# Optimization experiments

Hardware: AMD Instinct MI355X
Metric: run time of the kernel (lower is better)

## Reference

```python
import jax, jax.numpy as jnp
import numpy as np

B, S, D = 2, 2048, 512
E, H, TOP_K = 8, 1024, 2
SCALE = 1.0


def setup_inputs() -> dict:
    key = jax.random.key(0)
    ks = jax.random.split(key, 7)
    s = lambda fan_in: 1.0 / np.sqrt(fan_in)
    return {
        "x": jax.random.normal(ks[0], (B, S, D), dtype=jnp.float32),
        "gate_w": jax.random.normal(ks[1], (E, D), dtype=jnp.float32) * s(D),
        "w1": jax.random.normal(ks[2], (E, H, D), dtype=jnp.float32) * s(D),
        "w2": jax.random.normal(ks[3], (E, D, H), dtype=jnp.float32) * s(H),
        "sg_gate": jax.random.normal(ks[4], (H, D), dtype=jnp.float32) * s(D),
        "sg_up": jax.random.normal(ks[5], (H, D), dtype=jnp.float32) * s(D),
        "sg_down": jax.random.normal(ks[6], (D, H), dtype=jnp.float32) * s(H),
    }


def reference(x, gate_w, w1, w2, sg_gate, sg_up, sg_down):
    b, s_len, d = x.shape
    xf = x.reshape(-1, d)                      # [N, D]
    n = xf.shape[0]

    # --- TopKRouter: logits -> top-k -> softmax over the k selected logits ---
    logits = (xf @ gate_w.T) * SCALE           # [N, E]
    topk_w, idx = jax.lax.top_k(logits, TOP_K)  # [N, K]
    topk_w = jax.nn.softmax(topk_w, axis=-1)
    # per-token combine weights scattered to expert slots: [N, E]
    comb = jnp.zeros((n, E), dtype=xf.dtype).at[jnp.arange(n)[:, None], idx].add(topk_w)

    # --- Routed experts (dense masked compute; weight 0 for unrouted) ---
    h = jax.nn.silu(jnp.einsum('td,ehd->teh', xf, w1))   # [N, E, H]
    eo = jnp.einsum('teh,edh->ted', h, w2)               # [N, E, D]
    routed = jnp.einsum('te,ted->td', comb, eo)          # [N, D]

    # --- Shared expert (SwiGLU), n_shared_experts = 1 ---
    shared = (jax.nn.silu(xf @ sg_gate.T) * (xf @ sg_up.T)) @ sg_down.T

    return (routed + shared).reshape(b, s_len, d)
```

## Files before the change

### kernel.cpp

```cpp
#include <hip/hip_runtime.h>
#include <hip/hip_bf16.h>


#define NTOK 4096
#define DDIM 512
#define HDIM 1024
#define NEXP 8
#define CAP  4096

typedef unsigned short u16;
typedef __attribute__((ext_vector_type(8))) short short8;
typedef __attribute__((ext_vector_type(4))) float f32x4;

__device__ __forceinline__ u16 f2bf(float f) {
  unsigned u = __float_as_uint(f);
  u += 0x7fffu + ((u >> 16) & 1u);
  return (u16)(u >> 16);
}
__device__ __forceinline__ float bf2f(u16 v) {
  return __uint_as_float(((unsigned)v) << 16);
}
__device__ __forceinline__ float silu_f(float v) { return v / (1.0f + __expf(-v)); }

__device__ __forceinline__ void gload16(const u16* g, u16* l) {
  __builtin_amdgcn_global_load_lds((const __attribute__((address_space(1))) void*)g,
                                   (__attribute__((address_space(3))) void*)l, 16, 0, 0);
}

__global__ __launch_bounds__(256) void prep(
    const float* __restrict__ x,   const float* __restrict__ gw,
    const float* __restrict__ w1,  const float* __restrict__ w2,
    const float* __restrict__ sgg, const float* __restrict__ sgu,
    const float* __restrict__ sgd,
    u16* __restrict__ Xb, u16* __restrict__ W1b, u16* __restrict__ W2b,
    u16* __restrict__ SGGb, u16* __restrict__ SGUb, u16* __restrict__ SGDb,
    int* __restrict__ tIdx, float2* __restrict__ tW) {
  if (blockIdx.x < NTOK / 4) {
    const int lane = threadIdx.x & 63;
    const int wid  = threadIdx.x >> 6;
    const int t = blockIdx.x * 4 + wid;
    const float4* xr = (const float4*)(x + (size_t)t * DDIM + lane * 8);
    const float4 x0 = xr[0], x1 = xr[1];
    short8 xbv;
    xbv[0]=f2bf(x0.x); xbv[1]=f2bf(x0.y); xbv[2]=f2bf(x0.z); xbv[3]=f2bf(x0.w);
    xbv[4]=f2bf(x1.x); xbv[5]=f2bf(x1.y); xbv[6]=f2bf(x1.z); xbv[7]=f2bf(x1.w);
    *(short8*)&Xb[(size_t)t * DDIM + lane * 8] = xbv;
    float p[NEXP];
#pragma unroll
    for (int e = 0; e < NEXP; ++e) {
      const float4* gr = (const float4*)(gw + (size_t)e * DDIM + lane * 8);
      const float4 g0 = gr[0], g1 = gr[1];
      p[e] = x0.x*g0.x + x0.y*g0.y + x0.z*g0.z + x0.w*g0.w +
             x1.x*g1.x + x1.y*g1.y + x1.z*g1.z + x1.w*g1.w;
    }
#pragma unroll
    for (int e = 0; e < NEXP; ++e) {
#pragma unroll
      for (int m = 32; m >= 1; m >>= 1) p[e] += __shfl_xor(p[e], m);
    }
    if (lane == 0) {
      int i0 = 0; float v0 = p[0];
#pragma unroll
      for (int e = 1; e < NEXP; ++e) if (p[e] > v0) { v0 = p[e]; i0 = e; }
      int i1 = -1; float v1 = -3.0e38f;
#pragma unroll
      for (int e = 0; e < NEXP; ++e) if (e != i0 && p[e] > v1) { v1 = p[e]; i1 = e; }
      const float ex1 = __expf(v1 - v0);
      const float inv = 1.0f / (1.0f + ex1);
      tIdx[t] = i0 | (i1 << 4);
      tW[t] = make_float2(inv, ex1 * inv);
    }
  } else {
    constexpr int NW1 = NEXP * HDIM * DDIM / 4;
    constexpr int NSG = HDIM * DDIM / 4;
    constexpr int TOT = 2 * NW1 + 3 * NSG;
    int i = (blockIdx.x - NTOK / 4) * 256 + threadIdx.x;
    const int stride = (gridDim.x - NTOK / 4) * 256;
    for (; i < TOT; i += stride) {
      const float* s; u16* d; int j = i;
      if (j < NW1)               { s = w1;  d = W1b;  }
      else if ((j -= NW1) < NW1) { s = w2;  d = W2b;  }
      else if ((j -= NW1) < NSG) { s = sgg; d = SGGb; }
      else if ((j -= NSG) < NSG) { s = sgu; d = SGUb; }
      else        { j -= NSG;      s = sgd; d = SGDb; }
      float4 v = ((const float4*)s)[j];
      ushort4 o;
      o.x = f2bf(v.x); o.y = f2bf(v.y); o.z = f2bf(v.z); o.w = f2bf(v.w);
      ((ushort4*)d)[j] = o;
    }
  }
}

__global__ __launch_bounds__(256) void build_lists(
    const int* __restrict__ tIdx,
    int* __restrict__ counts, int* __restrict__ elist) {
  const int e = blockIdx.x;
  __shared__ int cnt;
  if (threadIdx.x == 0) cnt = 0;
  __syncthreads();
  const int lane = threadIdx.x & 63;
  int* el = elist + e * CAP;
  for (int base = 0; base < NTOK; base += 256) {
    const int t = base + threadIdx.x;
    const int pk = tIdx[t];
#pragma unroll
    for (int slot = 0; slot < 2; ++slot) {
      const bool m = (((pk >> (slot * 4)) & 15) == e);
      const unsigned long long b = __ballot(m);
      const int my  = __popcll(b & ((1ull << lane) - 1));
      const int tot = __popcll(b);
      int wbase = 0;
      if (lane == 0 && tot) wbase = atomicAdd(&cnt, tot);
      wbase = __shfl(wbase, 0);
      if (m) el[wbase + my] = t * 2 + slot;
    }
  }
  __syncthreads();
  if (threadIdx.x == 0) counts[e] = cnt;
}

#define BUFE (128 * 32)

__global__ __launch_bounds__(512, 6) void gemm_up(
    const u16* __restrict__ Xb, const u16* __restrict__ W1b,
    const u16* __restrict__ SGGb, const u16* __restrict__ SGUb,
    u16* __restrict__ Hbuf, u16* __restrict__ ACT,
    const int* __restrict__ counts, const int* __restrict__ elist) {
  constexpr int KDIM = DDIM, KSTEP = KDIM / 32;
  const int z = blockIdx.z;
  const int m0 = blockIdx.y * 128;
  const bool routed = (z < NEXP);

  int mlim; const u16* Bp = nullptr; const int* lst = nullptr;
  if (routed) {
    if (blockIdx.x >= 8) return;
    mlim = counts[z];
    lst = elist + z * CAP;
    Bp = W1b + (size_t)z * HDIM * KDIM;
  } else {
    mlim = NTOK;
  }
  if (m0 >= mlim) return;

  __shared__ __align__(16) u16 As[3 * BUFE];
  __shared__ __align__(16) u16 Bs[3 * BUFE];
  __shared__ int rowE[128];

  const int tid = threadIdx.x;
  const int wid = tid >> 6, lane = tid & 63;

  if (routed) {
    if (tid < 128) {
      int idx = m0 + tid; if (idx > mlim - 1) idx = mlim - 1;
      rowE[tid] = lst[idx];
    }
    __syncthreads();
  }

  const int row = tid >> 2;
  const int kcp = ((tid & 3) - ((row >> 1) & 3)) & 3;
  const int arow = routed ? (rowE[row] >> 1) : (m0 + row);
  const u16* aG = Xb + (size_t)arow * KDIM + kcp * 8;
  const u16* bG;
  if (routed) {
    bG = Bp + (size_t)(blockIdx.x * 128 + row) * KDIM + kcp * 8;
  } else {
    const int n0 = blockIdx.x * 64;
    bG = (row < 64) ? SGGb + (size_t)(n0 + row) * KDIM + kcp * 8
                    : SGUb + (size_t)(n0 + row - 64) * KDIM + kcp * 8;
  }

  const int lr = lane & 15, lk = lane >> 4;
  const int rslot = ((lk + ((lr >> 1) & 3)) & 3) * 8;

  auto STAGE = [&](int kt, int c) {
    gload16(aG + kt * 32, As + c * BUFE + tid * 8);
    gload16(bG + kt * 32, Bs + c * BUFE + tid * 8);
  };

  const f32x4 zero = {0.f, 0.f, 0.f, 0.f};

  if (routed) {
    const int n0 = blockIdx.x * 128;
    const int wm = (wid >> 2) * 64, wn = (wid & 3) * 32;
    f32x4 acc[4][2];
#pragma unroll
    for (int i = 0; i < 4; ++i)
#pragma unroll
      for (int j = 0; j < 2; ++j) acc[i][j] = zero;

    STAGE(0, 0); STAGE(1, 1);
    for (int kt = 0; kt < KSTEP; ++kt) {
      if (kt + 1 < KSTEP) asm volatile("s_waitcnt vmcnt(2)" ::: "memory");
      else                asm volatile("s_waitcnt vmcnt(0)" ::: "memory");
      __builtin_amdgcn_s_barrier();
      __builtin_amdgcn_sched_barrier(0);
      if (kt + 2 < KSTEP) STAGE(kt + 2, (kt + 2) % 3);
      const u16* ab = As + (kt % 3) * BUFE;
      const u16* bb = Bs + (kt % 3) * BUFE;
      short8 a[4], b[2];
#pragma unroll
      for (int i = 0; i < 4; ++i)
        a[i] = *(const short8*)&ab[(wm + i * 16 + lr) * 32 + rslot];
#pragma unroll
      for (int j = 0; j < 2; ++j)
        b[j] = *(const short8*)&bb[(wn + j * 16 + lr) * 32 + rslot];
      __builtin_amdgcn_s_setprio(1);
#pragma unroll
      for (int i = 0; i < 4; ++i)
#pragma unroll
        for (int j = 0; j < 2; ++j)
          acc[i][j] = __builtin_amdgcn_mfma_f32_16x16x32_bf16(a[i], b[j], acc[i][j], 0, 0, 0);
      __builtin_amdgcn_s_setprio(0);
    }

#pragma unroll
    for (int i = 0; i < 4; ++i) {
#pragma unroll
      for (int j = 0; j < 2; ++j) {
        const int col = n0 + wn + j * 16 + lr;
#pragma unroll
        for (int r = 0; r < 4; ++r) {
          const int m = wm + i * 16 + lk * 4 + r;
          if (m0 + m < mlim)
            Hbuf[(size_t)rowE[m] * HDIM + col] = f2bf(silu_f(acc[i][j][r]));
        }
      }
    }
  } else {
    const int n0 = blockIdx.x * 64;
    const int wm = (wid >> 2) * 64, ws = (wid & 3) * 16;
    f32x4 ag[4], au[4];
#pragma unroll
    for (int i = 0; i < 4; ++i) { ag[i] = zero; au[i] = zero; }

    STAGE(0, 0); STAGE(1, 1);
    for (int kt = 0; kt < KSTEP; ++kt) {
      if (kt + 1 < KSTEP) asm volatile("s_waitcnt vmcnt(2)" ::: "memory");
      else                asm volatile("s_waitcnt vmcnt(0)" ::: "memory");
      __builtin_amdgcn_s_barrier();
      __builtin_amdgcn_sched_barrier(0);
      if (kt + 2 < KSTEP) STAGE(kt + 2, (kt + 2) % 3);
      const u16* ab = As + (kt % 3) * BUFE;
      const u16* bb = Bs + (kt % 3) * BUFE;
      short8 a[4], bg, bu;
#pragma unroll
      for (int i = 0; i < 4; ++i)
        a[i] = *(const short8*)&ab[(wm + i * 16 + lr) * 32 + rslot];
      bg = *(const short8*)&bb[(ws + lr) * 32 + rslot];
      bu = *(const short8*)&bb[(64 + ws + lr) * 32 + rslot];
      __builtin_amdgcn_s_setprio(1);
#pragma unroll
      for (int i = 0; i < 4; ++i) {
        ag[i] = __builtin_amdgcn_mfma_f32_16x16x32_bf16(a[i], bg, ag[i], 0, 0, 0);
        au[i] = __builtin_amdgcn_mfma_f32_16x16x32_bf16(a[i], bu, au[i], 0, 0, 0);
      }
      __builtin_amdgcn_s_setprio(0);
    }

#pragma unroll
    for (int i = 0; i < 4; ++i) {
      const int col = n0 + ws + lr;
#pragma unroll
      for (int r = 0; r < 4; ++r) {
        const int m = wm + i * 16 + lk * 4 + r;
        ACT[(size_t)(m0 + m) * HDIM + col] = f2bf(silu_f(ag[i][r]) * au[i][r]);
      }
    }
  }
}

__global__ __launch_bounds__(512, 6) void gemm_down(
    const u16* __restrict__ Hbuf, const u16* __restrict__ W2b,
    const u16* __restrict__ ACT,  const u16* __restrict__ SGDb,
    u16* __restrict__ eo0, u16* __restrict__ eo1,
    float* __restrict__ sh0, float* __restrict__ sh1,
    const int* __restrict__ counts, const int* __restrict__ elist) {
  constexpr int KFULL = HDIM;
  constexpr int KSTEP = 512 / 32;
  const int z = blockIdx.z;
  const int n0 = blockIdx.x * 128;
  const int m0 = blockIdx.y * 128;
  const bool routed = (z < 2 * NEXP);
  const int khalf = routed ? (z & 1) : (z - 2 * NEXP);
  const int koff = khalf * 512;

  int mlim; const u16* Ap; const u16* Bp; const int* lst = nullptr;
  if (routed) {
    const int e = z >> 1;
    mlim = counts[e];
    lst = elist + e * CAP;
    Ap = Hbuf;
    Bp = W2b + (size_t)e * DDIM * KFULL;
  } else {
    mlim = NTOK;
    Ap = ACT;
    Bp = SGDb;
  }
  if (m0 >= mlim) return;

  __shared__ __align__(16) u16 As[3 * BUFE];
  __shared__ __align__(16) u16 Bs[3 * BUFE];
  __shared__ int rowE[128];

  const int tid = threadIdx.x;
  const int wid = tid >> 6, lane = tid & 63;

  if (routed) {
    if (tid < 128) {
      int idx = m0 + tid; if (idx > mlim - 1) idx = mlim - 1;
      rowE[tid] = lst[idx];
    }
    __syncthreads();
  }

  const int row = tid >> 2;
  const int kcp = ((tid & 3) - ((row >> 1) & 3)) & 3;
  const int arow = routed ? rowE[row] : (m0 + row);
  const u16* aG = Ap + (size_t)arow * KFULL + koff + kcp * 8;
  const u16* bG = Bp + (size_t)(n0 + row) * KFULL + koff + kcp * 8;

  const int wm = (wid >> 2) * 64, wn = (wid & 3) * 32;
  const int lr = lane & 15, lk = lane >> 4;
  const int rslot = ((lk + ((lr >> 1) & 3)) & 3) * 8;

  const f32x4 zero = {0.f, 0.f, 0.f, 0.f};
  f32x4 acc[4][2];
#pragma unroll
  for (int i = 0; i < 4; ++i)
#pragma unroll
    for (int j = 0; j < 2; ++j) acc[i][j] = zero;

  auto STAGE = [&](int kt, int c) {
    gload16(aG + kt * 32, As + c * BUFE + tid * 8);
    gload16(bG + kt * 32, Bs + c * BUFE + tid * 8);
  };

  STAGE(0, 0); STAGE(1, 1);
  for (int kt = 0; kt < KSTEP; ++kt) {
    if (kt + 1 < KSTEP) asm volatile("s_waitcnt vmcnt(2)" ::: "memory");
    else                asm volatile("s_waitcnt vmcnt(0)" ::: "memory");
    __builtin_amdgcn_s_barrier();
    __builtin_amdgcn_sched_barrier(0);
    if (kt + 2 < KSTEP) STAGE(kt + 2, (kt + 2) % 3);
    const u16* ab = As + (kt % 3) * BUFE;
    const u16* bb = Bs + (kt % 3) * BUFE;
    short8 a[4], b[2];
#pragma unroll
    for (int i = 0; i < 4; ++i)
      a[i] = *(const short8*)&ab[(wm + i * 16 + lr) * 32 + rslot];
#pragma unroll
    for (int j = 0; j < 2; ++j)
      b[j] = *(const short8*)&bb[(wn + j * 16 + lr) * 32 + rslot];
    __builtin_amdgcn_s_setprio(1);
#pragma unroll
    for (int i = 0; i < 4; ++i)
#pragma unroll
      for (int j = 0; j < 2; ++j)
        acc[i][j] = __builtin_amdgcn_mfma_f32_16x16x32_bf16(a[i], b[j], acc[i][j], 0, 0, 0);
    __builtin_amdgcn_s_setprio(0);
  }

#pragma unroll
  for (int i = 0; i < 4; ++i) {
#pragma unroll
    for (int j = 0; j < 2; ++j) {
      const int col = n0 + wn + j * 16 + lr;
#pragma unroll
      for (int r = 0; r < 4; ++r) {
        const int m = wm + i * 16 + lk * 4 + r;
        if (routed) {
          if (m0 + m < mlim) {
            u16* dst = khalf ? eo1 : eo0;
            dst[(size_t)rowE[m] * DDIM + col] = f2bf(acc[i][j][r]);
          }
        } else {
          float* dst = khalf ? sh1 : sh0;
          dst[(size_t)(m0 + m) * DDIM + col] = acc[i][j][r];
        }
      }
    }
  }
}

__global__ __launch_bounds__(256) void combine_kernel(
    const u16* __restrict__ eo0, const u16* __restrict__ eo1,
    const float* __restrict__ sh0, const float* __restrict__ sh1,
    const float2* __restrict__ tW, float* __restrict__ out) {
  const int g = blockIdx.x * 256 + threadIdx.x;
  const int t = g >> 6;
  const int c0 = (g & 63) * 8;
  const float2 w = tW[t];
  const size_t r0 = (size_t)(t * 2) * DDIM + c0;
  const size_t r1 = (size_t)(t * 2 + 1) * DDIM + c0;
  const short8 a0 = *(const short8*)&eo0[r0];
  const short8 a1 = *(const short8*)&eo0[r1];
  const short8 b0 = *(const short8*)&eo1[r0];
  const short8 b1 = *(const short8*)&eo1[r1];
  const size_t so = (size_t)t * DDIM + c0;
  const float4 s0a = ((const float4*)(sh0 + so))[0];
  const float4 s0b = ((const float4*)(sh0 + so))[1];
  const float4 s1a = ((const float4*)(sh1 + so))[0];
  const float4 s1b = ((const float4*)(sh1 + so))[1];
  float o[8];
  o[0]=s0a.x+s1a.x; o[1]=s0a.y+s1a.y; o[2]=s0a.z+s1a.z; o[3]=s0a.w+s1a.w;
  o[4]=s0b.x+s1b.x; o[5]=s0b.y+s1b.y; o[6]=s0b.z+s1b.z; o[7]=s0b.w+s1b.w;
#pragma unroll
  for (int k = 0; k < 8; ++k)
    o[k] += w.x * (bf2f((u16)a0[k]) + bf2f((u16)b0[k])) +
            w.y * (bf2f((u16)a1[k]) + bf2f((u16)b1[k]));
  float4 v0 = {o[0], o[1], o[2], o[3]};
  float4 v1 = {o[4], o[5], o[6], o[7]};
  ((float4*)(out + so))[0] = v0;
  ((float4*)(out + so))[1] = v1;
}

extern "C" void kernel_launch(void* const* d_in, const int* in_sizes, int n_in,
                              void* d_out, int out_size, void* d_ws, size_t ws_size,
                              hipStream_t stream) {
  const float* x    = (const float*)d_in[0];
  const float* gw   = (const float*)d_in[1];
  const float* w1   = (const float*)d_in[2];
  const float* w2   = (const float*)d_in[3];
  const float* sgg  = (const float*)d_in[4];
  const float* sgu  = (const float*)d_in[5];
  const float* sgd  = (const float*)d_in[6];
  float* out = (float*)d_out;

  char* ws = (char*)d_ws;
  size_t off = 0;
  auto take = [&](size_t bytes) {
    size_t r = off; off += (bytes + 255) & ~(size_t)255; return r;
  };
  int*    counts = (int*)   (ws + take(NEXP * sizeof(int)));
  int*    elist  = (int*)   (ws + take((size_t)NEXP * CAP * sizeof(int)));
  int*    tIdx   = (int*)   (ws + take((size_t)NTOK * sizeof(int)));
  float2* tW     = (float2*)(ws + take((size_t)NTOK * sizeof(float2)));
  u16*    Xb     = (u16*)   (ws + take((size_t)NTOK * DDIM * 2));
  u16*    W1b    = (u16*)   (ws + take((size_t)NEXP * HDIM * DDIM * 2));
  u16*    W2b    = (u16*)   (ws + take((size_t)NEXP * DDIM * HDIM * 2));
  u16*    SGGb   = (u16*)   (ws + take((size_t)HDIM * DDIM * 2));
  u16*    SGUb   = (u16*)   (ws + take((size_t)HDIM * DDIM * 2));
  u16*    SGDb   = (u16*)   (ws + take((size_t)DDIM * HDIM * 2));
  u16*    Hbuf   = (u16*)   (ws + take((size_t)NTOK * 2 * HDIM * 2));
  u16*    ACT    = (u16*)   (ws + take((size_t)NTOK * HDIM * 2));
  u16*    eo0    = (u16*)   (ws + take((size_t)NTOK * 2 * DDIM * 2));
  u16*    eo1    = (u16*)   (ws + take((size_t)NTOK * 2 * DDIM * 2));
  float*  sh0    = (float*) (ws + take((size_t)NTOK * DDIM * 4));
  float*  sh1    = (float*) (ws + take((size_t)NTOK * DDIM * 4));
  if (off > ws_size) return;

  prep<<<dim3(3072), 256, 0, stream>>>(x, gw, w1, w2, sgg, sgu, sgd,
                                       Xb, W1b, W2b, SGGb, SGUb, SGDb, tIdx, tW);
  build_lists<<<NEXP, 256, 0, stream>>>(tIdx, counts, elist);
  gemm_up<<<dim3(16, 32, NEXP + 1), 512, 0, stream>>>(
      Xb, W1b, SGGb, SGUb, Hbuf, ACT, counts, elist);
  gemm_down<<<dim3(DDIM / 128, 32, 2 * NEXP + 2), 512, 0, stream>>>(
      Hbuf, W2b, ACT, SGDb, eo0, eo1, sh0, sh1, counts, elist);
  combine_kernel<<<NTOK * 64 / 256, 256, 0, stream>>>(eo0, eo1, sh0, sh1, tW, out);
}
```

Before: 106.2 us.

## Use persistent fixed-size grids with strided M-tile loops in expert GEMMs

Replaces the 3D grids, which launched many early-exiting blocks for empty expert tiles, with a flat 512-block grid per GEMM. Each routed block owns an (expert, N-tile, strip) and loops over M tiles with stride 4. Shared-expert blocks loop over two M tiles in gemm_up and one in gemm_down. This removes launch and scheduling overhead from idle blocks and balances the uneven per-expert token counts. The cost is a fixed amount of work per block, which can cause load imbalance when one expert receives many tokens.

```diff
diff --git a/kernel.cpp b/kernel.cpp
--- a/kernel.cpp
+++ b/kernel.cpp
@@ -127,68 +127,263 @@
     u16* __restrict__ Hbuf, u16* __restrict__ ACT,
     const int* __restrict__ counts, const int* __restrict__ elist) {
   constexpr int KDIM = DDIM, KSTEP = KDIM / 32;
-  const int z = blockIdx.z;
-  const int m0 = blockIdx.y * 128;
-  const bool routed = (z < NEXP);
-
-  int mlim; const u16* Bp = nullptr; const int* lst = nullptr;
-  if (routed) {
-    if (blockIdx.x >= 8) return;
-    mlim = counts[z];
-    lst = elist + z * CAP;
-    Bp = W1b + (size_t)z * HDIM * KDIM;
-  } else {
-    mlim = NTOK;
-  }
-  if (m0 >= mlim) return;
+  const int h = blockIdx.x;
+  const int tid = threadIdx.x;
+  const int wid = tid >> 6, lane = tid & 63;
+  const int row = tid >> 2;
+  const int kcp = ((tid & 3) - ((row >> 1) & 3)) & 3;
+  const int lr = lane & 15, lk = lane >> 4;
+  const int rslot = ((lk + ((lr >> 1) & 3)) & 3) * 8;
 
   __shared__ __align__(16) u16 As[3 * BUFE];
   __shared__ __align__(16) u16 Bs[3 * BUFE];
   __shared__ int rowE[128];
 
+  const f32x4 zero = {0.f, 0.f, 0.f, 0.f};
+
+  if (h < 256) {
+    const int e = h >> 5;
+    const int nx = h & 7, strip = (h >> 3) & 3;
+    const int mlim = counts[e];
+    const int* lst = elist + e * CAP;
+    const u16* Bp = W1b + (size_t)e * HDIM * KDIM;
+    const u16* bG = Bp + (size_t)(nx * 128 + row) * KDIM + kcp * 8;
+    const int n0 = nx * 128;
+    const int wm = (wid >> 2) * 64, wn = (wid & 3) * 32;
+
+    for (int mt = strip; mt * 128 < mlim; mt += 4) {
+      const int m0 = mt * 128;
+      __syncthreads();
+      if (tid < 128) {
+        int idx = m0 + tid; if (idx > mlim - 1) idx = mlim - 1;
+        rowE[tid] = lst[idx];
+      }
+      __syncthreads();
+      const u16* aG = Xb + (size_t)(rowE[row] >> 1) * KDIM + kcp * 8;
+
+      f32x4 acc[4][2];
+#pragma unroll
+      for (int i = 0; i < 4; ++i)
+#pragma unroll
+        for (int j = 0; j < 2; ++j) acc[i][j] = zero;
+
+      auto STAGE = [&](int kt, int c) {
+        gload16(aG + kt * 32, As + c * BUFE + tid * 8);
+        gload16(bG + kt * 32, Bs + c * BUFE + tid * 8);
+      };
+      STAGE(0, 0); STAGE(1, 1);
+      for (int kt = 0; kt < KSTEP; ++kt) {
+        if (kt + 1 < KSTEP) asm volatile("s_waitcnt vmcnt(2)" ::: "memory");
+        else                asm volatile("s_waitcnt vmcnt(0)" ::: "memory");
+        __builtin_amdgcn_s_barrier();
+        __builtin_amdgcn_sched_barrier(0);
+        if (kt + 2 < KSTEP) STAGE(kt + 2, (kt + 2) % 3);
+        const u16* ab = As + (kt % 3) * BUFE;
+        const u16* bb = Bs + (kt % 3) * BUFE;
+        short8 a[4], b[2];
+#pragma unroll
+        for (int i = 0; i < 4; ++i)
+          a[i] = *(const short8*)&ab[(wm + i * 16 + lr) * 32 + rslot];
+#pragma unroll
+        for (int j = 0; j < 2; ++j)
+          b[j] = *(const short8*)&bb[(wn + j * 16 + lr) * 32 + rslot];
+        __builtin_amdgcn_s_setprio(1);
+#pragma unroll
+        for (int i = 0; i < 4; ++i)
+#pragma unroll
+          for (int j = 0; j < 2; ++j)
+            acc[i][j] = __builtin_amdgcn_mfma_f32_16x16x32_bf16(a[i], b[j], acc[i][j], 0, 0, 0);
+        __builtin_amdgcn_s_setprio(0);
+      }
+
+#pragma unroll
+      for (int i = 0; i < 4; ++i) {
+#pragma unroll
+        for (int j = 0; j < 2; ++j) {
+          const int col = n0 + wn + j * 16 + lr;
+#pragma unroll
+          for (int r = 0; r < 4; ++r) {
+            const int m = wm + i * 16 + lk * 4 + r;
+            if (m0 + m < mlim)
+              Hbuf[(size_t)rowE[m] * HDIM + col] = f2bf(silu_f(acc[i][j][r]));
+          }
+        }
+      }
+    }
+  } else {
+    const int s = h - 256;
+    const int nx = s & 15, mstrip = s >> 4;
+    const int n0 = nx * 64;
+    const u16* bG = (row < 64)
+        ? SGGb + (size_t)(n0 + row) * KDIM + kcp * 8
+        : SGUb + (size_t)(n0 + row - 64) * KDIM + kcp * 8;
+    const int wm = (wid >> 2) * 64, ws = (wid & 3) * 16;
+
+    for (int mt = mstrip; mt < 32; mt += 16) {
+      const int m0 = mt * 128;
+      __syncthreads();
+      const u16* aG = Xb + (size_t)(m0 + row) * KDIM + kcp * 8;
+
+      f32x4 ag[4], au[4];
+#pragma unroll
+      for (int i = 0; i < 4; ++i) { ag[i] = zero; au[i] = zero; }
+
+      auto STAGE = [&](int kt, int c) {
+        gload16(aG + kt * 32, As + c * BUFE + tid * 8);
+        gload16(bG + kt * 32, Bs + c * BUFE + tid * 8);
+      };
+      STAGE(0, 0); STAGE(1, 1);
+      for (int kt = 0; kt < KSTEP; ++kt) {
+        if (kt + 1 < KSTEP) asm volatile("s_waitcnt vmcnt(2)" ::: "memory");
+        else                asm volatile("s_waitcnt vmcnt(0)" ::: "memory");
+        __builtin_amdgcn_s_barrier();
+        __builtin_amdgcn_sched_barrier(0);
+        if (kt + 2 < KSTEP) STAGE(kt + 2, (kt + 2) % 3);
+        const u16* ab = As + (kt % 3) * BUFE;
+        const u16* bb = Bs + (kt % 3) * BUFE;
+        short8 a[4], bg, bu;
+#pragma unroll
+        for (int i = 0; i < 4; ++i)
+          a[i] = *(const short8*)&ab[(wm + i * 16 + lr) * 32 + rslot];
+        bg = *(const short8*)&bb[(ws + lr) * 32 + rslot];
+        bu = *(const short8*)&bb[(64 + ws + lr) * 32 + rslot];
+        __builtin_amdgcn_s_setprio(1);
+#pragma unroll
+        for (int i = 0; i < 4; ++i) {
+          ag[i] = __builtin_amdgcn_mfma_f32_16x16x32_bf16(a[i], bg, ag[i], 0, 0, 0);
+          au[i] = __builtin_amdgcn_mfma_f32_16x16x32_bf16(a[i], bu, au[i], 0, 0, 0);
+        }
+        __builtin_amdgcn_s_setprio(0);
+      }
+
+#pragma unroll
+      for (int i = 0; i < 4; ++i) {
+        const int col = n0 + ws + lr;
+#pragma unroll
+        for (int r = 0; r < 4; ++r) {
+          const int m = wm + i * 16 + lk * 4 + r;
+          ACT[(size_t)(m0 + m) * HDIM + col] = f2bf(silu_f(ag[i][r]) * au[i][r]);
+        }
+      }
+    }
+  }
+}
+
+__global__ __launch_bounds__(512, 6) void gemm_down(
+    const u16* __restrict__ Hbuf, const u16* __restrict__ W2b,
+    const u16* __restrict__ ACT,  const u16* __restrict__ SGDb,
+    u16* __restrict__ eo0, u16* __restrict__ eo1,
+    float* __restrict__ sh0, float* __restrict__ sh1,
+    const int* __restrict__ counts, const int* __restrict__ elist) {
+  constexpr int KFULL = HDIM;
+  constexpr int KSTEP = 512 / 32;
+  const int h = blockIdx.x;
   const int tid = threadIdx.x;
   const int wid = tid >> 6, lane = tid & 63;
-
-  if (routed) {
-    if (tid < 128) {
-      int idx = m0 + tid; if (idx > mlim - 1) idx = mlim - 1;
-      rowE[tid] = lst[idx];
-    }
-    __syncthreads();
-  }
-
   const int row = tid >> 2;
   const int kcp = ((tid & 3) - ((row >> 1) & 3)) & 3;
-  const int arow = routed ? (rowE[row] >> 1) : (m0 + row);
-  const u16* aG = Xb + (size_t)arow * KDIM + kcp * 8;
-  const u16* bG;
-  if (routed) {
-    bG = Bp + (size_t)(blockIdx.x * 128 + row) * KDIM + kcp * 8;
-  } else {
-    const int n0 = blockIdx.x * 64;
-    bG = (row < 64) ? SGGb + (size_t)(n0 + row) * KDIM + kcp * 8
-                    : SGUb + (size_t)(n0 + row - 64) * KDIM + kcp * 8;
-  }
-
   const int lr = lane & 15, lk = lane >> 4;
   const int rslot = ((lk + ((lr >> 1) & 3)) & 3) * 8;
-
-  auto STAGE = [&](int kt, int c) {
-    gload16(aG + kt * 32, As + c * BUFE + tid * 8);
-    gload16(bG + kt * 32, Bs + c * BUFE + tid * 8);
-  };
+  const int wm = (wid >> 2) * 64, wn = (wid & 3) * 32;
+
+  __shared__ __align__(16) u16 As[3 * BUFE];
+  __shared__ __align__(16) u16 Bs[3 * BUFE];
+  __shared__ int rowE[128];
 
   const f32x4 zero = {0.f, 0.f, 0.f, 0.f};
 
-  if (routed) {
-    const int n0 = blockIdx.x * 128;
-    const int wm = (wid >> 2) * 64, wn = (wid & 3) * 32;
+  if (h < 256) {
+    const int ek = h >> 4;
+    const int e = ek >> 1, khalf = ek & 1;
+    const int nx = h & 3, strip = (h >> 2) & 3;
+    const int koff = khalf * 512;
+    const int mlim = counts[e];
+    const int* lst = elist + e * CAP;
+    const u16* Bp = W2b + (size_t)e * DDIM * KFULL;
+    const u16* bG = Bp + (size_t)(nx * 128 + row) * KFULL + koff + kcp * 8;
+    const int n0 = nx * 128;
+    u16* dst = khalf ? eo1 : eo0;
+
+    for (int mt = strip; mt * 128 < mlim; mt += 4) {
+      const int m0 = mt * 128;
+      __syncthreads();
+      if (tid < 128) {
+        int idx = m0 + tid; if (idx > mlim - 1) idx = mlim - 1;
+        rowE[tid] = lst[idx];
+      }
+      __syncthreads();
+      const u16* aG = Hbuf + (size_t)rowE[row] * KFULL + koff + kcp * 8;
+
+      f32x4 acc[4][2];
+#pragma unroll
+      for (int i = 0; i < 4; ++i)
+#pragma unroll
+        for (int j = 0; j < 2; ++j) acc[i][j] = zero;
+
+      auto STAGE = [&](int kt, int c) {
+        gload16(aG + kt * 32, As + c * BUFE + tid * 8);
+        gload16(bG + kt * 32, Bs + c * BUFE + tid * 8);
+      };
+      STAGE(0, 0); STAGE(1, 1);
+      for (int kt = 0; kt < KSTEP; ++kt) {
+        if (kt + 1 < KSTEP) asm volatile("s_waitcnt vmcnt(2)" ::: "memory");
+        else                asm volatile("s_waitcnt vmcnt(0)" ::: "memory");
+        __builtin_amdgcn_s_barrier();
+        __builtin_amdgcn_sched_barrier(0);
+        if (kt + 2 < KSTEP) STAGE(kt + 2, (kt + 2) % 3);
+        const u16* ab = As + (kt % 3) * BUFE;
+        const u16* bb = Bs + (kt % 3) * BUFE;
+        short8 a[4], b[2];
+#pragma unroll
+        for (int i = 0; i < 4; ++i)
+          a[i] = *(const short8*)&ab[(wm + i * 16 + lr) * 32 + rslot];
+#pragma unroll
+        for (int j = 0; j < 2; ++j)
+          b[j] = *(const short8*)&bb[(wn + j * 16 + lr) * 32 + rslot];
+        __builtin_amdgcn_s_setprio(1);
+#pragma unroll
+        for (int i = 0; i < 4; ++i)
+#pragma unroll
+          for (int j = 0; j < 2; ++j)
+            acc[i][j] = __builtin_amdgcn_mfma_f32_16x16x32_bf16(a[i], b[j], acc[i][j], 0, 0, 0);
+        __builtin_amdgcn_s_setprio(0);
+      }
+
+#pragma unroll
+      for (int i = 0; i < 4; ++i) {
+#pragma unroll
+        for (int j = 0; j < 2; ++j) {
+          const int col = n0 + wn + j * 16 + lr;
+#pragma unroll
+          for (int r = 0; r < 4; ++r) {
+            const int m = wm + i * 16 + lk * 4 + r;
+            if (m0 + m < mlim)
+              dst[(size_t)rowE[m] * DDIM + col] = f2bf(acc[i][j][r]);
+          }
+        }
+      }
+    }
+  } else {
+    const int s = h - 256;
+    const int khalf = s >> 7;
+    const int nx = s & 3, mt = (s >> 2) & 31;
+    const int koff = khalf * 512;
+    const int n0 = nx * 128;
+    const int m0 = mt * 128;
+    float* dst = khalf ? sh1 : sh0;
+    const u16* aG = ACT  + (size_t)(m0 + row) * KFULL + koff + kcp * 8;
+    const u16* bG = SGDb + (size_t)(n0 + row) * KFULL + koff + kcp * 8;
+
     f32x4 acc[4][2];
 #pragma unroll
     for (int i = 0; i < 4; ++i)
 #pragma unroll
       for (int j = 0; j < 2; ++j) acc[i][j] = zero;
 
+    auto STAGE = [&](int kt, int c) {
+      gload16(aG + kt * 32, As + c * BUFE + tid * 8);
+      gload16(bG + kt * 32, Bs + c * BUFE + tid * 8);
+    };
     STAGE(0, 0); STAGE(1, 1);
     for (int kt = 0; kt < KSTEP; ++kt) {
       if (kt + 1 < KSTEP) asm volatile("s_waitcnt vmcnt(2)" ::: "memory");
@@ -222,160 +417,6 @@
 #pragma unroll
         for (int r = 0; r < 4; ++r) {
           const int m = wm + i * 16 + lk * 4 + r;
-          if (m0 + m < mlim)
-            Hbuf[(size_t)rowE[m] * HDIM + col] = f2bf(silu_f(acc[i][j][r]));
-        }
-      }
-    }
-  } else {
-    const int n0 = blockIdx.x * 64;
-    const int wm = (wid >> 2) * 64, ws = (wid & 3) * 16;
-    f32x4 ag[4], au[4];
-#pragma unroll
-    for (int i = 0; i < 4; ++i) { ag[i] = zero; au[i] = zero; }
-
-    STAGE(0, 0); STAGE(1, 1);
-    for (int kt = 0; kt < KSTEP; ++kt) {
-      if (kt + 1 < KSTEP) asm volatile("s_waitcnt vmcnt(2)" ::: "memory");
-      else                asm volatile("s_waitcnt vmcnt(0)" ::: "memory");
-      __builtin_amdgcn_s_barrier();
-      __builtin_amdgcn_sched_barrier(0);
-      if (kt + 2 < KSTEP) STAGE(kt + 2, (kt + 2) % 3);
-      const u16* ab = As + (kt % 3) * BUFE;
-      const u16* bb = Bs + (kt % 3) * BUFE;
-      short8 a[4], bg, bu;
-#pragma unroll
-      for (int i = 0; i < 4; ++i)
-        a[i] = *(const short8*)&ab[(wm + i * 16 + lr) * 32 + rslot];
-      bg = *(const short8*)&bb[(ws + lr) * 32 + rslot];
-      bu = *(const short8*)&bb[(64 + ws + lr) * 32 + rslot];
-      __builtin_amdgcn_s_setprio(1);
-#pragma unroll
-      for (int i = 0; i < 4; ++i) {
-        ag[i] = __builtin_amdgcn_mfma_f32_16x16x32_bf16(a[i], bg, ag[i], 0, 0, 0);
-        au[i] = __builtin_amdgcn_mfma_f32_16x16x32_bf16(a[i], bu, au[i], 0, 0, 0);
-      }
-      __builtin_amdgcn_s_setprio(0);
-    }
-
-#pragma unroll
-    for (int i = 0; i < 4; ++i) {
-      const int col = n0 + ws + lr;
-#pragma unroll
-      for (int r = 0; r < 4; ++r) {
-        const int m = wm + i * 16 + lk * 4 + r;
-        ACT[(size_t)(m0 + m) * HDIM + col] = f2bf(silu_f(ag[i][r]) * au[i][r]);
-      }
-    }
-  }
-}
-
-__global__ __launch_bounds__(512, 6) void gemm_down(
-    const u16* __restrict__ Hbuf, const u16* __restrict__ W2b,
-    const u16* __restrict__ ACT,  const u16* __restrict__ SGDb,
-    u16* __restrict__ eo0, u16* __restrict__ eo1,
-    float* __restrict__ sh0, float* __restrict__ sh1,
-    const int* __restrict__ counts, const int* __restrict__ elist) {
-  constexpr int KFULL = HDIM;
-  constexpr int KSTEP = 512 / 32;
-  const int z = blockIdx.z;
-  const int n0 = blockIdx.x * 128;
-  const int m0 = blockIdx.y * 128;
-  const bool routed = (z < 2 * NEXP);
-  const int khalf = routed ? (z & 1) : (z - 2 * NEXP);
-  const int koff = khalf * 512;
-
-  int mlim; const u16* Ap; const u16* Bp; const int* lst = nullptr;
-  if (routed) {
-    const int e = z >> 1;
-    mlim = counts[e];
-    lst = elist + e * CAP;
-    Ap = Hbuf;
-    Bp = W2b + (size_t)e * DDIM * KFULL;
-  } else {
-    mlim = NTOK;
-    Ap = ACT;
-    Bp = SGDb;
-  }
-  if (m0 >= mlim) return;
-
-  __shared__ __align__(16) u16 As[3 * BUFE];
-  __shared__ __align__(16) u16 Bs[3 * BUFE];
-  __shared__ int rowE[128];
-
-  const int tid = threadIdx.x;
-  const int wid = tid >> 6, lane = tid & 63;
-
-  if (routed) {
-    if (tid < 128) {
-      int idx = m0 + tid; if (idx > mlim - 1) idx = mlim - 1;
-      rowE[tid] = lst[idx];
-    }
-    __syncthreads();
-  }
-
-  const int row = tid >> 2;
-  const int kcp = ((tid & 3) - ((row >> 1) & 3)) & 3;
-  const int arow = routed ? rowE[row] : (m0 + row);
-  const u16* aG = Ap + (size_t)arow * KFULL + koff + kcp * 8;
-  const u16* bG = Bp + (size_t)(n0 + row) * KFULL + koff + kcp * 8;
-
-  const int wm = (wid >> 2) * 64, wn = (wid & 3) * 32;
-  const int lr = lane & 15, lk = lane >> 4;
-  const int rslot = ((lk + ((lr >> 1) & 3)) & 3) * 8;
-
-  const f32x4 zero = {0.f, 0.f, 0.f, 0.f};
-  f32x4 acc[4][2];
-#pragma unroll
-  for (int i = 0; i < 4; ++i)
-#pragma unroll
-    for (int j = 0; j < 2; ++j) acc[i][j] = zero;
-
-  auto STAGE = [&](int kt, int c) {
-    gload16(aG + kt * 32, As + c * BUFE + tid * 8);
-    gload16(bG + kt * 32, Bs + c * BUFE + tid * 8);
-  };
-
-  STAGE(0, 0); STAGE(1, 1);
-  for (int kt = 0; kt < KSTEP; ++kt) {
-    if (kt + 1 < KSTEP) asm volatile("s_waitcnt vmcnt(2)" ::: "memory");
-    else                asm volatile("s_waitcnt vmcnt(0)" ::: "memory");
-    __builtin_amdgcn_s_barrier();
-    __builtin_amdgcn_sched_barrier(0);
-    if (kt + 2 < KSTEP) STAGE(kt + 2, (kt + 2) % 3);
-    const u16* ab = As + (kt % 3) * BUFE;
-    const u16* bb = Bs + (kt % 3) * BUFE;
-    short8 a[4], b[2];
-#pragma unroll
-    for (int i = 0; i < 4; ++i)
-      a[i] = *(const short8*)&ab[(wm + i * 16 + lr) * 32 + rslot];
-#pragma unroll
-    for (int j = 0; j < 2; ++j)
-      b[j] = *(const short8*)&bb[(wn + j * 16 + lr) * 32 + rslot];
-    __builtin_amdgcn_s_setprio(1);
-#pragma unroll
-    for (int i = 0; i < 4; ++i)
-#pragma unroll
-      for (int j = 0; j < 2; ++j)
-        acc[i][j] = __builtin_amdgcn_mfma_f32_16x16x32_bf16(a[i], b[j], acc[i][j], 0, 0, 0);
-    __builtin_amdgcn_s_setprio(0);
-  }
-
-#pragma unroll
-  for (int i = 0; i < 4; ++i) {
-#pragma unroll
-    for (int j = 0; j < 2; ++j) {
-      const int col = n0 + wn + j * 16 + lr;
-#pragma unroll
-      for (int r = 0; r < 4; ++r) {
-        const int m = wm + i * 16 + lk * 4 + r;
-        if (routed) {
-          if (m0 + m < mlim) {
-            u16* dst = khalf ? eo1 : eo0;
-            dst[(size_t)rowE[m] * DDIM + col] = f2bf(acc[i][j][r]);
-          }
-        } else {
-          float* dst = khalf ? sh1 : sh0;
           dst[(size_t)(m0 + m) * DDIM + col] = acc[i][j][r];
         }
       }
@@ -453,9 +494,9 @@
   prep<<<dim3(3072), 256, 0, stream>>>(x, gw, w1, w2, sgg, sgu, sgd,
                                        Xb, W1b, W2b, SGGb, SGUb, SGDb, tIdx, tW);
   build_lists<<<NEXP, 256, 0, stream>>>(tIdx, counts, elist);
-  gemm_up<<<dim3(16, 32, NEXP + 1), 512, 0, stream>>>(
+  gemm_up<<<dim3(512), 512, 0, stream>>>(
       Xb, W1b, SGGb, SGUb, Hbuf, ACT, counts, elist);
-  gemm_down<<<dim3(DDIM / 128, 32, 2 * NEXP + 2), 512, 0, stream>>>(
+  gemm_down<<<dim3(512), 512, 0, stream>>>(
       Hbuf, W2b, ACT, SGDb, eo0, eo1, sh0, sh1, counts, elist);
   combine_kernel<<<NTOK * 64 / 256, 256, 0, stream>>>(eo0, eo1, sh0, sh1, tW, out);
 }
```

New measurement: 137.9 us. +29.9%, slower.
